# Kernel optimization log

Measured on AMD Instinct MI355X. Metric: run time of the kernel, lower is better.

The kernel has to match this reference:

```python
import jax, jax.numpy as jnp
import numpy as np

SCALES = (64, 64, 64)  # (Dx, Dy, Dz)
B = 32


def _rev_gridding(grid, scales):
    """Reverse gridding (GRNet gridding.rev_forward): for each voxel cell
    (x,y,z) with x,y,z >= 1, the output point is the weighted centroid of the
    cell's 8 corner vertices, weighted by the grid values at those vertices,
    then re-centered by scale/2 per axis. Cells on the x==0/y==0/z==0 border
    or with zero total corner weight produce the zero point.
    grid: (B, Dx*Dy*Dz) flattened with x fastest (j = z*Dy*Dx + y*Dx + x).
    returns ptcloud: (B, Dx*Dy*Dz, 3) in voxel-centered units.
    """
    Dx, Dy, Dz = scales
    b = grid.shape[0]
    G = grid.reshape(b, Dz, Dy, Dx)
    # 8 corners of each interior cell; each view has shape (B, Dz-1, Dy-1, Dx-1)
    c000 = G[:, :-1, :-1, :-1]; c001 = G[:, :-1, :-1, 1:]
    c010 = G[:, :-1, 1:, :-1]; c011 = G[:, :-1, 1:, 1:]
    c100 = G[:, 1:, :-1, :-1]; c101 = G[:, 1:, :-1, 1:]
    c110 = G[:, 1:, 1:, :-1]; c111 = G[:, 1:, 1:, 1:]
    wsum = c000 + c001 + c010 + c011 + c100 + c101 + c110 + c111
    wx1 = c001 + c011 + c101 + c111  # corners at the +x face
    wy1 = c010 + c011 + c110 + c111  # corners at the +y face
    wz1 = c100 + c101 + c110 + c111  # corners at the +z face
    valid = wsum > 0
    inv = jnp.where(valid, 1.0, 0.0) / jnp.where(valid, wsum, 1.0)  # safe 1/wsum
    x = jnp.arange(1, Dx, dtype=grid.dtype)                 # (Dx-1,)
    y = jnp.arange(1, Dy, dtype=grid.dtype)[:, None]        # (Dy-1, 1)
    z = jnp.arange(1, Dz, dtype=grid.dtype)[:, None, None]  # (Dz-1, 1, 1)
    half = lambda d: jnp.asarray(d, grid.dtype) / 2
    px = jnp.where(valid, ((x - 1) * wsum + wx1) * inv - half(Dx), 0.0)
    py = jnp.where(valid, ((y - 1) * wsum + wy1) * inv - half(Dy), 0.0)
    pz = jnp.where(valid, ((z - 1) * wsum + wz1) * inv - half(Dz), 0.0)
    pad = ((0, 0), (1, 0), (1, 0), (1, 0))  # zero points on the x/y/z == 0 borders
    pts = jnp.stack([jnp.pad(px, pad), jnp.pad(py, pad), jnp.pad(pz, pad)], axis=-1)
    return pts.reshape(b, -1, 3)


def setup_inputs() -> dict:
    key = jax.random.key(0)
    Dx, Dy, Dz = SCALES
    grid = jax.random.uniform(key, (B, Dx * Dy * Dz), dtype=jnp.float32)
    return {"grid": grid}


def reference(grid) -> jnp.ndarray:
    Dx, Dy, Dz = SCALES
    ptcloud = _rev_gridding(grid, SCALES)
    scaling = jnp.asarray([2.0 / Dx, 2.0 / Dy, 2.0 / Dz], dtype=grid.dtype)
    return ptcloud * scaling  # broadcast over (B, N, 3) -> coords in [-1, 1]
```

## Files before the change

kernel.cpp:

```cpp
#include <hip/hip_runtime.h>


#define DX 64
#define DY 64
#define DZ 64

__global__ __launch_bounds__(256)
void GriddingReverse_kernel(const float* __restrict__ grid,
                            float* __restrict__ out,
                            int total)
{
    int idx = blockIdx.x * blockDim.x + threadIdx.x;
    if (idx >= total) return;

    int x = idx & (DX - 1);
    int y = (idx >> 6) & (DY - 1);
    int z = (idx >> 12) & (DZ - 1);
    int b = idx >> 18;

    float ox = 0.0f, oy = 0.0f, oz = 0.0f;

    if (x > 0 && y > 0 && z > 0) {
        const float* __restrict__ g = grid + ((size_t)b << 18);
        int base = ((z - 1) << 12) + ((y - 1) << 6) + (x - 1);
        float c000 = g[base];
        float c001 = g[base + 1];
        float c010 = g[base + DX];
        float c011 = g[base + DX + 1];
        float c100 = g[base + DX * DY];
        float c101 = g[base + DX * DY + 1];
        float c110 = g[base + DX * DY + DX];
        float c111 = g[base + DX * DY + DX + 1];

        float wsum = ((c000 + c001) + (c010 + c011)) + ((c100 + c101) + (c110 + c111));
        if (wsum > 0.0f) {
            float inv = 1.0f / wsum;
            float wx1 = (c001 + c011) + (c101 + c111);
            float wy1 = (c010 + c011) + (c110 + c111);
            float wz1 = (c100 + c101) + (c110 + c111);
            const float s = 2.0f / 64.0f;
            ox = ((float)(x - 1) + wx1 * inv - 32.0f) * s;
            oy = ((float)(y - 1) + wy1 * inv - 32.0f) * s;
            oz = ((float)(z - 1) + wz1 * inv - 32.0f) * s;
        }
    }

    size_t o = (size_t)idx * 3;
    out[o]     = ox;
    out[o + 1] = oy;
    out[o + 2] = oz;
}

extern "C" void kernel_launch(void* const* d_in, const int* in_sizes, int n_in,
                              void* d_out, int out_size, void* d_ws, size_t ws_size,
                              hipStream_t stream)
{
    const float* grid = (const float*)d_in[0];
    float* out = (float*)d_out;
    int total = in_sizes[0];
    int block = 256;
    int ngrid = (total + block - 1) / block;
    GriddingReverse_kernel<<<ngrid, block, 0, stream>>>(grid, out, total);
}
```

Before: 28.60 us.

## Process four x-adjacent cells per thread with float4 loads and stores

Each thread now handles four consecutive x cells. It loads four rows as float4 plus one scalar left neighbour per row, and shares the partial corner sums between adjacent cells. Outputs are written as three float4 stores instead of strided scalar stores. This cuts redundant global loads and the instruction count per point, in exchange for fewer threads and a kernel that assumes the total size is divisible by four.

```diff
diff --git a/kernel.cpp b/kernel.cpp
--- a/kernel.cpp
+++ b/kernel.cpp
@@ -1,54 +1,78 @@
 #include <hip/hip_runtime.h>
 
-
-#define DX 64
-#define DY 64
-#define DZ 64
 
 __global__ __launch_bounds__(256)
 void GriddingReverse_kernel(const float* __restrict__ grid,
                             float* __restrict__ out,
-                            int total)
+                            int nthreads)
 {
-    int idx = blockIdx.x * blockDim.x + threadIdx.x;
-    if (idx >= total) return;
+    int tid = blockIdx.x * blockDim.x + threadIdx.x;
+    if (tid >= nthreads) return;
 
-    int x = idx & (DX - 1);
-    int y = (idx >> 6) & (DY - 1);
-    int z = (idx >> 12) & (DZ - 1);
-    int b = idx >> 18;
+    int idx0 = tid << 2;
+    int x0 = idx0 & 63;
+    int y  = (idx0 >> 6) & 63;
+    int z  = (idx0 >> 12) & 63;
+    int b  = idx0 >> 18;
 
-    float ox = 0.0f, oy = 0.0f, oz = 0.0f;
+    float px[4] = {0.f, 0.f, 0.f, 0.f};
+    float py[4] = {0.f, 0.f, 0.f, 0.f};
+    float pz[4] = {0.f, 0.f, 0.f, 0.f};
 
-    if (x > 0 && y > 0 && z > 0) {
+    if (y > 0 && z > 0) {
         const float* __restrict__ g = grid + ((size_t)b << 18);
-        int base = ((z - 1) << 12) + ((y - 1) << 6) + (x - 1);
-        float c000 = g[base];
-        float c001 = g[base + 1];
-        float c010 = g[base + DX];
-        float c011 = g[base + DX + 1];
-        float c100 = g[base + DX * DY];
-        float c101 = g[base + DX * DY + 1];
-        float c110 = g[base + DX * DY + DX];
-        float c111 = g[base + DX * DY + DX + 1];
+        int rA = ((z - 1) << 12) + ((y - 1) << 6);
+        int rB = rA + 64;
+        int rC = rA + 4096;
+        int rD = rC + 64;
 
-        float wsum = ((c000 + c001) + (c010 + c011)) + ((c100 + c101) + (c110 + c111));
-        if (wsum > 0.0f) {
-            float inv = 1.0f / wsum;
-            float wx1 = (c001 + c011) + (c101 + c111);
-            float wy1 = (c010 + c011) + (c110 + c111);
-            float wz1 = (c100 + c101) + (c110 + c111);
-            const float s = 2.0f / 64.0f;
-            ox = ((float)(x - 1) + wx1 * inv - 32.0f) * s;
-            oy = ((float)(y - 1) + wy1 * inv - 32.0f) * s;
-            oz = ((float)(z - 1) + wz1 * inv - 32.0f) * s;
+        float4 qA = *reinterpret_cast<const float4*>(g + rA + x0);
+        float4 qB = *reinterpret_cast<const float4*>(g + rB + x0);
+        float4 qC = *reinterpret_cast<const float4*>(g + rC + x0);
+        float4 qD = *reinterpret_cast<const float4*>(g + rD + x0);
+        float mA = 0.f, mB = 0.f, mC = 0.f, mD = 0.f;
+        if (x0 > 0) {
+            mA = g[rA + x0 - 1];
+            mB = g[rB + x0 - 1];
+            mC = g[rC + x0 - 1];
+            mD = g[rD + x0 - 1];
+        }
+
+        float aV[5] = {mA, qA.x, qA.y, qA.z, qA.w};
+        float bV[5] = {mB, qB.x, qB.y, qB.z, qB.w};
+        float cV[5] = {mC, qC.x, qC.y, qC.z, qC.w};
+        float dV[5] = {mD, qD.x, qD.y, qD.z, qD.w};
+
+        float s[5], u[5], v[5];
+        #pragma unroll
+        for (int k = 0; k < 5; ++k) {
+            u[k] = bV[k] + dV[k];
+            v[k] = cV[k] + dV[k];
+            s[k] = (aV[k] + bV[k]) + v[k];
+        }
+
+        const float sc = 2.0f / 64.0f;
+        float fy = (float)(y - 1) - 32.0f;
+        float fz = (float)(z - 1) - 32.0f;
+        #pragma unroll
+        for (int i = 0; i < 4; ++i) {
+            int x = x0 + i;
+            if (x > 0) {
+                float wsum = s[i] + s[i + 1];
+                if (wsum > 0.0f) {
+                    float inv = 1.0f / wsum;
+                    px[i] = ((float)(x - 1) - 32.0f + s[i + 1] * inv) * sc;
+                    py[i] = (fy + (u[i] + u[i + 1]) * inv) * sc;
+                    pz[i] = (fz + (v[i] + v[i + 1]) * inv) * sc;
+                }
+            }
         }
     }
 
-    size_t o = (size_t)idx * 3;
-    out[o]     = ox;
-    out[o + 1] = oy;
-    out[o + 2] = oz;
+    float4* op = reinterpret_cast<float4*>(out + (size_t)idx0 * 3);
+    op[0] = make_float4(px[0], py[0], pz[0], px[1]);
+    op[1] = make_float4(py[1], pz[1], px[2], py[2]);
+    op[2] = make_float4(pz[2], px[3], py[3], pz[3]);
 }
 
 extern "C" void kernel_launch(void* const* d_in, const int* in_sizes, int n_in,
@@ -58,7 +82,8 @@
     const float* grid = (const float*)d_in[0];
     float* out = (float*)d_out;
     int total = in_sizes[0];
+    int nthreads = total >> 2;
     int block = 256;
-    int ngrid = (total + block - 1) / block;
-    GriddingReverse_kernel<<<ngrid, block, 0, stream>>>(grid, out, total);
+    int ngrid = (nthreads + block - 1) / block;
+    GriddingReverse_kernel<<<ngrid, block, 0, stream>>>(grid, out, nthreads);
 }
```

Result: slower. 38.19 us (+33.5%).
